# Kernel tuning notes

Hardware: AMD Instinct MI355X
Metric: run time of the kernel (lower is better)

The kernel has to match this reference:

```python
import jax, jax.numpy as jnp
import numpy as np

T, N, E, F, H = 8, 50000, 800000, 128, 128
NHEADS = 4
DH = H // NHEADS


def setup_inputs() -> dict:
    key = jax.random.key(0)
    ks = jax.random.split(key, 24)

    def rn(k, shape, scale=0.05):
        return jax.random.normal(k, shape, dtype=jnp.float32) * scale

    return {
        "xs": rn(ks[0], (T, N, F), 1.0),
        "edge_index": jax.random.randint(ks[1], (T, 2, E), 0, N, dtype=jnp.int32),
        # SAGEConv layers: out = mean_aggr(x_src) @ Wl + x @ Wr + b (bias on lin_l only)
        "Wl1": rn(ks[2], (F, H)), "Wr1": rn(ks[3], (F, H)), "b1": jnp.zeros((H,), jnp.float32),
        "Wl2": rn(ks[4], (H, H)), "Wr2": rn(ks[5], (H, H)), "b2": jnp.zeros((H,), jnp.float32),
        "Wl3": rn(ks[6], (H, H)), "Wr3": rn(ks[7], (H, H)), "b3": jnp.zeros((H,), jnp.float32),
        # MultiheadAttention (applied as x @ W, i.e. W = torch_weight.T)
        "Wq": rn(ks[8], (H, H)), "bq": jnp.zeros((H,), jnp.float32),
        "Wk": rn(ks[9], (H, H)), "bk": jnp.zeros((H,), jnp.float32),
        "Wv": rn(ks[10], (H, H)), "bv": jnp.zeros((H,), jnp.float32),
        "Wo": rn(ks[11], (H, H)), "bo": jnp.zeros((H,), jnp.float32),
        # MLP head
        "Wh1": rn(ks[12], (H, H // 2)), "bh1": jnp.zeros((H // 2,), jnp.float32),
        "Wh2": rn(ks[13], (H // 2, 1)), "bh2": jnp.zeros((1,), jnp.float32),
    }


def _sage(x, src, dst, Wl, Wr, b):
    # gather messages from source nodes, mean-aggregate at destinations
    msg = x[src]                                               # [E, F]
    ssum = jax.ops.segment_sum(msg, dst, num_segments=N)       # [N, F]
    cnt = jax.ops.segment_sum(jnp.ones((msg.shape[0],), x.dtype), dst, num_segments=N)
    agg = ssum / jnp.maximum(cnt, 1.0)[:, None]
    return agg @ Wl + x @ Wr + b


def reference(xs, edge_index, Wl1, Wr1, b1, Wl2, Wr2, b2, Wl3, Wr3, b3,
              Wq, bq, Wk, bk, Wv, bv, Wo, bo, Wh1, bh1, Wh2, bh2):
    def step(_, xe):
        x, ei = xe
        src, dst = ei[0], ei[1]
        h = jax.nn.relu(_sage(x, src, dst, Wl1, Wr1, b1))  # dropout = identity (eval)
        h = jax.nn.relu(_sage(h, src, dst, Wl2, Wr2, b2))
        h = jax.nn.relu(_sage(h, src, dst, Wl3, Wr3, b3))
        return None, h.mean(axis=0)                        # mean pool over nodes -> [H]

    _, pooled = jax.lax.scan(step, None, (xs, edge_index))  # [T, H]

    seq = pooled[None]                                      # [1, T, H]
    q = (seq @ Wq + bq).reshape(1, T, NHEADS, DH).transpose(0, 2, 1, 3)
    k = (seq @ Wk + bk).reshape(1, T, NHEADS, DH).transpose(0, 2, 1, 3)
    v = (seq @ Wv + bv).reshape(1, T, NHEADS, DH).transpose(0, 2, 1, 3)
    scale = jnp.float32(1.0 / np.sqrt(DH))
    attn = jax.nn.softmax(jnp.einsum('bhqd,bhkd->bhqk', q, k) * scale, axis=-1)
    o = jnp.einsum('bhqk,bhkd->bhqd', attn, v).transpose(0, 2, 1, 3).reshape(1, T, H)
    o = o @ Wo + bo                                         # [1, T, H]

    z = o[:, -1, :]                                         # [1, H] (last timestep)
    h1 = jax.nn.relu(z @ Wh1 + bh1)
    logits = jax.nn.sigmoid(h1 @ Wh2 + bh2)                 # [1, 1]
    return logits.squeeze(-1)                               # [1]
```

## Files before the change

kernel.cpp:

```cpp
#include <hip/hip_runtime.h>
#include <math.h>

#define TT 8
#define NN 50000
#define EE 800000
#define FF 128
#define HH 128

#define NB 98
#define BSHIFT 9
#define CAP 14336
#define RS 16384

typedef __attribute__((ext_vector_type(8))) short short8;
typedef __attribute__((ext_vector_type(4))) float f32x4;
typedef __attribute__((ext_vector_type(2))) float f32x2;
typedef unsigned char uchar;

__device__ inline unsigned bf16pack(float x) {
    unsigned u = __float_as_uint(x);
    return (u + 0x7fffu + ((u >> 16) & 1u)) >> 16;
}
__device__ inline unsigned pack2bf16_trunc(float lo, float hi) {
    return (__float_as_uint(hi) & 0xffff0000u) | (__float_as_uint(lo) >> 16);
}


__global__ __launch_bounds__(256) void cast_x_kernel(const float4* __restrict__ in,
                                                     int* __restrict__ out, long n4) {
    long i = (long)blockIdx.x * 256 + threadIdx.x;
    if (i < n4) {
        float4 v = in[i];
        int w = __builtin_amdgcn_cvt_pk_fp8_f32(v.x, v.y, 0, false);
        w = __builtin_amdgcn_cvt_pk_fp8_f32(v.z, v.w, w, true);
        out[i] = w;
    }
}

__global__ __launch_bounds__(256) void wprep_kernel(const float* __restrict__ Wl,
                                                    const float* __restrict__ Wr,
                                                    ushort* __restrict__ Bt) {
    int n = blockIdx.x;
    int k = threadIdx.x;
    float v = (k < 128) ? Wl[k * HH + n] : Wr[(k - 128) * HH + n];
    Bt[n * 256 + k] = (ushort)bf16pack(v);
}


__global__ __launch_bounds__(256) void partA_kernel(const int* __restrict__ ei,
                                                    int* __restrict__ bucketCursor,
                                                    uint2* __restrict__ pairs) {
    __shared__ int hist[NB];
    __shared__ int base[NB];
    int t = blockIdx.y, tid = threadIdx.x;
    const int* src = ei + (size_t)t * 2 * EE;
    const int* dst = src + EE;
    int e0 = blockIdx.x * 2048;
    int s[8], d[8];
#pragma unroll
    for (int k = 0; k < 8; k++) {
        int e = e0 + k * 256 + tid;
        bool ok = e < EE;
        s[k] = ok ? src[e] : -1;
        d[k] = ok ? dst[e] : -1;
    }
    if (tid < NB) hist[tid] = 0;
    __syncthreads();
#pragma unroll
    for (int k = 0; k < 8; k++)
        if (d[k] >= 0) atomicAdd(&hist[d[k] >> BSHIFT], 1);
    __syncthreads();
    if (tid < NB) {
        base[tid] = atomicAdd(&bucketCursor[t * NB + tid], hist[tid]);
        hist[tid] = 0;
    }
    __syncthreads();
#pragma unroll
    for (int k = 0; k < 8; k++)
        if (d[k] >= 0) {
            int b = d[k] >> BSHIFT;
            int idx = base[b] + atomicAdd(&hist[b], 1);
            if (idx < CAP)
                pairs[((size_t)t * NB + b) * RS + idx] = make_uint2((unsigned)s[k], (unsigned)d[k]);
        }
}

__global__ void bscan_kernel(const int* __restrict__ bucketCursor,
                             int* __restrict__ bucketBase) {
    int t = threadIdx.x;
    if (t < TT) {
        int run = 0;
        for (int b = 0; b < NB; b++) {
            bucketBase[t * NB + b] = run;
            int c = bucketCursor[t * NB + b];
            run += (c > CAP ? CAP : c);
        }
    }
}

__global__ __launch_bounds__(256) void partB_kernel(const uint2* __restrict__ pairs,
                                                    const int* __restrict__ bucketCursor,
                                                    const int* __restrict__ bucketBase,
                                                    int* __restrict__ cnt,
                                                    int* __restrict__ rowstart,
                                                    int* __restrict__ srcs_sorted) {
    __shared__ int hist[512];
    __shared__ int offs[512];
    __shared__ int sh2[256];
    __shared__ int staged[CAP];
    int t = blockIdx.y, b = blockIdx.x, tid = threadIdx.x;
    int n0 = b << BSHIFT;
    int nn = NN - n0; if (nn > 512) nn = 512;
    int cb = bucketCursor[t * NB + b]; if (cb > CAP) cb = CAP;
    int ebase = bucketBase[t * NB + b];
    const uint2* P = pairs + ((size_t)t * NB + b) * RS;

    hist[tid] = 0; hist[tid + 256] = 0;
    __syncthreads();
    for (int i = tid; i < cb; i += 256) atomicAdd(&hist[(int)P[i].y - n0], 1);
    __syncthreads();
    int a0 = hist[2 * tid], a1 = hist[2 * tid + 1];
    sh2[tid] = a0 + a1;
    __syncthreads();
    for (int off = 1; off < 256; off <<= 1) {
        int v = (tid >= off) ? sh2[tid - off] : 0;
        __syncthreads();
        sh2[tid] += v;
        __syncthreads();
    }
    int excl = sh2[tid] - (a0 + a1);
    offs[2 * tid] = excl;
    offs[2 * tid + 1] = excl + a0;
    __syncthreads();
    for (int i = tid; i < nn; i += 256) {
        cnt[(size_t)t * NN + n0 + i] = hist[i];
        rowstart[(size_t)t * NN + n0 + i] = ebase + offs[i];
    }
    __syncthreads();
    hist[tid] = offs[tid]; hist[tid + 256] = offs[tid + 256];
    __syncthreads();
    for (int i = tid; i < cb; i += 256) {
        uint2 p = P[i];
        int slot = atomicAdd(&hist[(int)p.y - n0], 1);
        staged[slot] = (int)p.x;
    }
    __syncthreads();
    int* outp = srcs_sorted + (size_t)t * EE + ebase;
    for (int i = tid; i < cb; i += 256) outp[i] = staged[i];
}

__global__ __launch_bounds__(256) void agg_kernel(const uchar* __restrict__ xin,
                                                  const int* __restrict__ srcs_sorted,
                                                  const int* __restrict__ rowstart,
                                                  const int* __restrict__ cnt,
                                                  uchar* __restrict__ aggq) {
    int node = blockIdx.x * 4 + (threadIdx.x >> 6);
    if (node >= NN) return;
    int lane = threadIdx.x & 63;
    int quad = lane >> 4, l15 = lane & 15;
    int rs = rowstart[node];
    int c = cnt[node];
    const uint2* x2 = (const uint2*)xin;
    float a0 = 0.f, a1 = 0.f, a2 = 0.f, a3 = 0.f, a4 = 0.f, a5 = 0.f, a6 = 0.f, a7 = 0.f;
    int j = quad;
    for (; j + 4 < c; j += 8) {
        int s0 = srcs_sorted[rs + j];
        int s1 = srcs_sorted[rs + j + 4];
        uint2 v0 = x2[(size_t)s0 * 16 + l15];
        uint2 v1 = x2[(size_t)s1 * 16 + l15];
        f32x2 p;
        p = __builtin_amdgcn_cvt_pk_f32_fp8((int)v0.x, false); a0 += p.x; a1 += p.y;
        p = __builtin_amdgcn_cvt_pk_f32_fp8((int)v0.x, true);  a2 += p.x; a3 += p.y;
        p = __builtin_amdgcn_cvt_pk_f32_fp8((int)v0.y, false); a4 += p.x; a5 += p.y;
        p = __builtin_amdgcn_cvt_pk_f32_fp8((int)v0.y, true);  a6 += p.x; a7 += p.y;
        p = __builtin_amdgcn_cvt_pk_f32_fp8((int)v1.x, false); a0 += p.x; a1 += p.y;
        p = __builtin_amdgcn_cvt_pk_f32_fp8((int)v1.x, true);  a2 += p.x; a3 += p.y;
        p = __builtin_amdgcn_cvt_pk_f32_fp8((int)v1.y, false); a4 += p.x; a5 += p.y;
        p = __builtin_amdgcn_cvt_pk_f32_fp8((int)v1.y, true);  a6 += p.x; a7 += p.y;
    }
    if (j < c) {
        uint2 v0 = x2[(size_t)srcs_sorted[rs + j] * 16 + l15];
        f32x2 p;
        p = __builtin_amdgcn_cvt_pk_f32_fp8((int)v0.x, false); a0 += p.x; a1 += p.y;
        p = __builtin_amdgcn_cvt_pk_f32_fp8((int)v0.x, true);  a2 += p.x; a3 += p.y;
        p = __builtin_amdgcn_cvt_pk_f32_fp8((int)v0.y, false); a4 += p.x; a5 += p.y;
        p = __builtin_amdgcn_cvt_pk_f32_fp8((int)v0.y, true);  a6 += p.x; a7 += p.y;
    }
#pragma unroll
    for (int o = 16; o <= 32; o <<= 1) {
        a0 += __shfl_xor(a0, o, 64);
        a1 += __shfl_xor(a1, o, 64);
        a2 += __shfl_xor(a2, o, 64);
        a3 += __shfl_xor(a3, o, 64);
        a4 += __shfl_xor(a4, o, 64);
        a5 += __shfl_xor(a5, o, 64);
        a6 += __shfl_xor(a6, o, 64);
        a7 += __shfl_xor(a7, o, 64);
    }
    if (quad == 0) {
        float inv = 1.0f / (float)(c > 0 ? c : 1);
        int w0 = __builtin_amdgcn_cvt_pk_fp8_f32(a0 * inv, a1 * inv, 0, false);
        w0 = __builtin_amdgcn_cvt_pk_fp8_f32(a2 * inv, a3 * inv, w0, true);
        int w1 = __builtin_amdgcn_cvt_pk_fp8_f32(a4 * inv, a5 * inv, 0, false);
        w1 = __builtin_amdgcn_cvt_pk_fp8_f32(a6 * inv, a7 * inv, w1, true);
        ((uint2*)aggq)[(size_t)node * 16 + l15] = make_uint2((unsigned)w0, (unsigned)w1);
    }
}

__global__ __launch_bounds__(256) void gemm_mfma_kernel(const uchar* __restrict__ AaggF,
                                                        const uchar* __restrict__ AxF,
                                                        const ushort* __restrict__ Bt,
                                                        const float* __restrict__ bias,
                                                        uchar* __restrict__ outF) {
    extern __shared__ char smem[];
    ushort* As = (ushort*)smem;
    ushort* Bs = (ushort*)(smem + 128 * 72 * 2);
    uchar* Cs = (uchar*)smem;

    size_t toff = (size_t)blockIdx.y * NN * HH;
    const uchar* Aagg = AaggF + toff;
    const uchar* Ax = AxF + toff;
    uchar* out = outF + toff;

    int tid = threadIdx.x;
    int row0 = blockIdx.x * 128;
    int lane = tid & 63, wave = tid >> 6;
    int wm = wave >> 1, wn = wave & 1;
    int l15 = lane & 15, quad = lane >> 4;

    f32x4 acc[4][4];
#pragma unroll
    for (int i = 0; i < 4; i++)
#pragma unroll
        for (int j = 0; j < 4; j++) acc[i][j] = (f32x4){0.f, 0.f, 0.f, 0.f};

    int srow = tid >> 1;
    int cb = (tid & 1) * 32;
    int grow = row0 + srow;

    for (int s = 0; s < 4; s++) {
        const uchar* Asrc = (s < 2) ? Aagg : Ax;
        int acol = (s & 1) * 64 + cb;
        uint4 r0 = make_uint4(0u, 0u, 0u, 0u), r1 = r0;
        if (grow < NN) {
            const uchar* ap = Asrc + (size_t)grow * HH + acol;
            r0 = *(const uint4*)ap;
            r1 = *(const uint4*)(ap + 16);
        }
        const ushort* bp = Bt + srow * 256 + s * 64 + cb;
        uint4 bv[4];
#pragma unroll
        for (int c = 0; c < 4; c++) bv[c] = *(const uint4*)(bp + c * 8);

        unsigned w[8] = {r0.x, r0.y, r0.z, r0.w, r1.x, r1.y, r1.z, r1.w};
        unsigned u[16];
#pragma unroll
        for (int wi = 0; wi < 8; wi++) {
            f32x2 lo = __builtin_amdgcn_cvt_pk_f32_fp8((int)w[wi], false);
            f32x2 hi = __builtin_amdgcn_cvt_pk_f32_fp8((int)w[wi], true);
            u[2 * wi] = pack2bf16_trunc(lo.x, lo.y);
            u[2 * wi + 1] = pack2bf16_trunc(hi.x, hi.y);
        }
        __syncthreads();
#pragma unroll
        for (int c = 0; c < 4; c++)
            *(uint4*)&As[srow * 72 + cb + c * 8] =
                make_uint4(u[4 * c], u[4 * c + 1], u[4 * c + 2], u[4 * c + 3]);
#pragma unroll
        for (int c = 0; c < 4; c++) *(uint4*)&Bs[srow * 72 + cb + c * 8] = bv[c];
        __syncthreads();
#pragma unroll
        for (int ks = 0; ks < 2; ks++) {
            int k0 = ks * 32 + quad * 8;
            short8 a[4], b[4];
#pragma unroll
            for (int i = 0; i < 4; i++)
                a[i] = *(const short8*)&As[(wm * 64 + i * 16 + l15) * 72 + k0];
#pragma unroll
            for (int j = 0; j < 4; j++)
                b[j] = *(const short8*)&Bs[(wn * 64 + j * 16 + l15) * 72 + k0];
#pragma unroll
            for (int i = 0; i < 4; i++)
#pragma unroll
                for (int j = 0; j < 4; j++)
                    acc[i][j] = __builtin_amdgcn_mfma_f32_16x16x32_bf16(a[i], b[j], acc[i][j], 0, 0, 0);
        }
    }
    __syncthreads();

#pragma unroll
    for (int i = 0; i < 4; i++)
#pragma unroll
        for (int j = 0; j < 4; j++) {
            int col = wn * 64 + j * 16 + l15;
            float bb = bias[col];
#pragma unroll
            for (int r = 0; r < 4; r++) {
                int rl = wm * 64 + i * 16 + quad * 4 + r;
                float v = fmaxf(acc[i][j][r] + bb, 0.f);
                int pk = __builtin_amdgcn_cvt_pk_fp8_f32(v, 0.f, 0, false);
                Cs[rl * 144 + col] = (uchar)(pk & 0xff);
            }
        }
    __syncthreads();

    int orow = tid >> 1;
    int ocb = (tid & 1) * 64;
    if (row0 + orow < NN) {
#pragma unroll
        for (int c = 0; c < 4; c++)
            *(uint4*)&out[(size_t)(row0 + orow) * HH + ocb + c * 16] =
                *(const uint4*)&Cs[orow * 144 + ocb + c * 16];
    }
}

__global__ __launch_bounds__(256) void pool_kernel(const uchar* __restrict__ hF,
                                                   float* __restrict__ pooled) {
    int t = blockIdx.y;
    const unsigned* h = (const unsigned*)(hF + (size_t)t * NN * HH);
    int tid = threadIdx.x;
    int wave = tid >> 6, lane = tid & 63;
    int fw = lane & 31;
    int rh = lane >> 5;
    float s0 = 0.f, s1 = 0.f, s2 = 0.f, s3 = 0.f;
    for (int r = blockIdx.x * 8 + wave * 2 + rh; r < NN; r += gridDim.x * 8) {
        unsigned u = h[(size_t)r * 32 + fw];
        f32x2 lo = __builtin_amdgcn_cvt_pk_f32_fp8((int)u, false);
        f32x2 hi = __builtin_amdgcn_cvt_pk_f32_fp8((int)u, true);
        s0 += lo.x; s1 += lo.y; s2 += hi.x; s3 += hi.y;
    }
    s0 += __shfl_xor(s0, 32, 64);
    s1 += __shfl_xor(s1, 32, 64);
    s2 += __shfl_xor(s2, 32, 64);
    s3 += __shfl_xor(s3, 32, 64);
    if (lane < 32) {
        const float inv = 1.0f / (float)NN;
        atomicAdd(&pooled[t * HH + fw * 4 + 0], s0 * inv);
        atomicAdd(&pooled[t * HH + fw * 4 + 1], s1 * inv);
        atomicAdd(&pooled[t * HH + fw * 4 + 2], s2 * inv);
        atomicAdd(&pooled[t * HH + fw * 4 + 3], s3 * inv);
    }
}

__global__ __launch_bounds__(256) void head_kernel(const float* __restrict__ pooled,
                                                   const float* __restrict__ Wq, const float* __restrict__ bq,
                                                   const float* __restrict__ Wk, const float* __restrict__ bk,
                                                   const float* __restrict__ Wv, const float* __restrict__ bv,
                                                   const float* __restrict__ Wo, const float* __restrict__ bo,
                                                   const float* __restrict__ Wh1, const float* __restrict__ bh1,
                                                   const float* __restrict__ Wh2, const float* __restrict__ bh2,
                                                   float* __restrict__ out) {
    __shared__ float seq[TT * HH];
    __shared__ float kb[TT * HH];
    __shared__ float vbuf[TT * HH];
    __shared__ float q7[HH];
    __shared__ float sc[4][8];
    __shared__ float zb[HH];
    __shared__ float ob[HH];
    __shared__ float h1b[64];
    int tid = threadIdx.x;
    for (int i = tid; i < TT * HH; i += 256) seq[i] = pooled[i];
    __syncthreads();
    for (int i = tid; i < TT * HH; i += 256) {
        int t = i >> 7, h = i & 127;
        float sk = bk[h], sv = bv[h];
        for (int j = 0; j < HH; j++) {
            float s = seq[t * HH + j];
            sk += s * Wk[j * HH + h];
            sv += s * Wv[j * HH + h];
        }
        kb[i] = sk;
        vbuf[i] = sv;
    }
    if (tid < HH) {
        float sq = bq[tid];
        for (int j = 0; j < HH; j++) sq += seq[7 * HH + j] * Wq[j * HH + tid];
        q7[tid] = sq;
    }
    __syncthreads();
    if (tid < 32) {
        int g = tid >> 3, tt = tid & 7;
        float s = 0.f;
        for (int d = 0; d < 32; d++) s += q7[g * 32 + d] * kb[tt * HH + g * 32 + d];
        sc[g][tt] = s * 0.1767766952966369f;
    }
    __syncthreads();
    if (tid < 4) {
        float m = -1e30f;
        for (int i = 0; i < 8; i++) m = fmaxf(m, sc[tid][i]);
        float e[8], sum = 0.f;
        for (int i = 0; i < 8; i++) { e[i] = expf(sc[tid][i] - m); sum += e[i]; }
        for (int i = 0; i < 8; i++) sc[tid][i] = e[i] / sum;
    }
    __syncthreads();
    if (tid < HH) {
        int g = tid >> 5;
        float s = 0.f;
        for (int t = 0; t < 8; t++) s += sc[g][t] * vbuf[t * HH + tid];
        zb[tid] = s;
    }
    __syncthreads();
    if (tid < HH) {
        float s = bo[tid];
        for (int j = 0; j < HH; j++) s += zb[j] * Wo[j * HH + tid];
        ob[tid] = s;
    }
    __syncthreads();
    if (tid < 64) {
        float s = bh1[tid];
        for (int j = 0; j < HH; j++) s += ob[j] * Wh1[j * 64 + tid];
        h1b[tid] = fmaxf(s, 0.f);
    }
    __syncthreads();
    if (tid == 0) {
        float s = bh2[0];
        for (int j = 0; j < 64; j++) s += h1b[j] * Wh2[j];
        out[0] = 1.0f / (1.0f + expf(-s));
    }
}


extern "C" void kernel_launch(void* const* d_in, const int* in_sizes, int n_in,
                              void* d_out, int out_size, void* d_ws, size_t ws_size,
                              hipStream_t stream) {
    const float* xs = (const float*)d_in[0];
    const int* ei = (const int*)d_in[1];
    const float* Wl1 = (const float*)d_in[2];
    const float* Wr1 = (const float*)d_in[3];
    const float* b1 = (const float*)d_in[4];
    const float* Wl2 = (const float*)d_in[5];
    const float* Wr2 = (const float*)d_in[6];
    const float* b2 = (const float*)d_in[7];
    const float* Wl3 = (const float*)d_in[8];
    const float* Wr3 = (const float*)d_in[9];
    const float* b3 = (const float*)d_in[10];
    const float* Wq = (const float*)d_in[11];
    const float* bq = (const float*)d_in[12];
    const float* Wk = (const float*)d_in[13];
    const float* bk = (const float*)d_in[14];
    const float* Wv = (const float*)d_in[15];
    const float* bv = (const float*)d_in[16];
    const float* Wo = (const float*)d_in[17];
    const float* bo = (const float*)d_in[18];
    const float* Wh1 = (const float*)d_in[19];
    const float* bh1 = (const float*)d_in[20];
    const float* Wh2 = (const float*)d_in[21];
    const float* bh2 = (const float*)d_in[22];

    size_t off = 0;
    char* base = (char*)d_ws;
    auto carve = [&](size_t bytes) -> char* {
        char* p = base + off;
        off += (bytes + 255) & ~(size_t)255;
        return p;
    };
    int* cnt = (int*)carve((size_t)TT * NN * 4);
    int* rowstart = (int*)carve((size_t)TT * NN * 4);
    int* srcs_sorted = (int*)carve((size_t)TT * EE * 4);
    int* bucketCursor = (int*)carve((size_t)TT * NB * 4);
    int* bucketBase = (int*)carve((size_t)TT * NB * 4);
    uint2* pairs = (uint2*)carve((size_t)TT * NB * RS * 8);
    uchar* xq = (uchar*)carve((size_t)TT * NN * HH);
    uchar* aggq = (uchar*)carve((size_t)TT * NN * HH);
    uchar* h1q = (uchar*)carve((size_t)TT * NN * HH);
    uchar* h2q = (uchar*)carve((size_t)TT * NN * HH);
    ushort* Bt1 = (ushort*)carve((size_t)128 * 256 * 2);
    ushort* Bt2 = (ushort*)carve((size_t)128 * 256 * 2);
    ushort* Bt3 = (ushort*)carve((size_t)128 * 256 * 2);
    float* pooled = (float*)carve((size_t)TT * HH * 4);

    hipMemsetAsync(pooled, 0, (size_t)TT * HH * 4, stream);
    hipMemsetAsync(bucketCursor, 0, (size_t)TT * NB * 4, stream);

    long n4 = (long)TT * NN * FF / 4;
    cast_x_kernel<<<(int)((n4 + 255) / 256), 256, 0, stream>>>((const float4*)xs, (int*)xq, n4);
    wprep_kernel<<<128, 256, 0, stream>>>(Wl1, Wr1, Bt1);
    wprep_kernel<<<128, 256, 0, stream>>>(Wl2, Wr2, Bt2);
    wprep_kernel<<<128, 256, 0, stream>>>(Wl3, Wr3, Bt3);

    partA_kernel<<<dim3((EE + 2047) / 2048, TT), 256, 0, stream>>>(ei, bucketCursor, pairs);
    bscan_kernel<<<1, 64, 0, stream>>>(bucketCursor, bucketBase);
    partB_kernel<<<dim3(NB, TT), 256, 0, stream>>>(pairs, bucketCursor, bucketBase,
                                                   cnt, rowstart, srcs_sorted);

    const int gemmGrid = (NN + 127) / 128;
    const int aggGrid = (NN + 3) / 4;
    const int gemmLds = 128 * 72 * 2 * 2;

    for (int t = 0; t < TT; t++)
        agg_kernel<<<aggGrid, 256, 0, stream>>>(xq + (size_t)t * NN * HH,
                                                srcs_sorted + (size_t)t * EE,
                                                rowstart + (size_t)t * NN,
                                                cnt + (size_t)t * NN,
                                                aggq + (size_t)t * NN * HH);
    gemm_mfma_kernel<<<dim3(gemmGrid, TT), 256, gemmLds, stream>>>(aggq, xq, Bt1, b1, h1q);
    for (int t = 0; t < TT; t++)
        agg_kernel<<<aggGrid, 256, 0, stream>>>(h1q + (size_t)t * NN * HH,
                                                srcs_sorted + (size_t)t * EE,
                                                rowstart + (size_t)t * NN,
                                                cnt + (size_t)t * NN,
                                                aggq + (size_t)t * NN * HH);
    gemm_mfma_kernel<<<dim3(gemmGrid, TT), 256, gemmLds, stream>>>(aggq, h1q, Bt2, b2, h2q);
    for (int t = 0; t < TT; t++)
        agg_kernel<<<aggGrid, 256, 0, stream>>>(h2q + (size_t)t * NN * HH,
                                                srcs_sorted + (size_t)t * EE,
                                                rowstart + (size_t)t * NN,
                                                cnt + (size_t)t * NN,
                                                aggq + (size_t)t * NN * HH);
    gemm_mfma_kernel<<<dim3(gemmGrid, TT), 256, gemmLds, stream>>>(aggq, h2q, Bt3, b3, h1q);

    pool_kernel<<<dim3(64, TT), 256, 0, stream>>>(h1q, pooled);

    head_kernel<<<1, 256, 0, stream>>>(pooled, Wq, bq, Wk, bk, Wv, bv, Wo, bo,
                                       Wh1, bh1, Wh2, bh2, (float*)d_out);
}
```

Baseline: 1.392 ms.

## Compress edge indices to 16-bit, batch agg launches over timesteps, split feature halves

```diff
diff --git a/kernel.cpp b/kernel.cpp
--- a/kernel.cpp
+++ b/kernel.cpp
@@ -37,19 +37,23 @@
     }
 }
 
-__global__ __launch_bounds__(256) void wprep_kernel(const float* __restrict__ Wl,
-                                                    const float* __restrict__ Wr,
+__global__ __launch_bounds__(256) void wprep_kernel(const float* __restrict__ Wl1, const float* __restrict__ Wr1,
+                                                    const float* __restrict__ Wl2, const float* __restrict__ Wr2,
+                                                    const float* __restrict__ Wl3, const float* __restrict__ Wr3,
                                                     ushort* __restrict__ Bt) {
+    int l = blockIdx.y;
+    const float* Wl = (l == 0) ? Wl1 : (l == 1) ? Wl2 : Wl3;
+    const float* Wr = (l == 0) ? Wr1 : (l == 1) ? Wr2 : Wr3;
     int n = blockIdx.x;
     int k = threadIdx.x;
     float v = (k < 128) ? Wl[k * HH + n] : Wr[(k - 128) * HH + n];
-    Bt[n * 256 + k] = (ushort)bf16pack(v);
+    Bt[(size_t)l * 128 * 256 + n * 256 + k] = (ushort)bf16pack(v);
 }
 
 
 __global__ __launch_bounds__(256) void partA_kernel(const int* __restrict__ ei,
                                                     int* __restrict__ bucketCursor,
-                                                    uint2* __restrict__ pairs) {
+                                                    unsigned* __restrict__ pairs) {
     __shared__ int hist[NB];
     __shared__ int base[NB];
     int t = blockIdx.y, tid = threadIdx.x;
@@ -81,7 +85,8 @@
             int b = d[k] >> BSHIFT;
             int idx = base[b] + atomicAdd(&hist[b], 1);
             if (idx < CAP)
-                pairs[((size_t)t * NB + b) * RS + idx] = make_uint2((unsigned)s[k], (unsigned)d[k]);
+                pairs[((size_t)t * NB + b) * RS + idx] =
+                    (unsigned)s[k] | ((unsigned)(d[k] & 511) << 16);
         }
 }
 
@@ -98,26 +103,26 @@
     }
 }
 
-__global__ __launch_bounds__(256) void partB_kernel(const uint2* __restrict__ pairs,
+__global__ __launch_bounds__(256) void partB_kernel(const unsigned* __restrict__ pairs,
                                                     const int* __restrict__ bucketCursor,
                                                     const int* __restrict__ bucketBase,
-                                                    int* __restrict__ cnt,
                                                     int* __restrict__ rowstart,
-                                                    int* __restrict__ srcs_sorted) {
+                                                    ushort* __restrict__ srcs_sorted) {
     __shared__ int hist[512];
     __shared__ int offs[512];
     __shared__ int sh2[256];
-    __shared__ int staged[CAP];
+    __shared__ ushort staged[CAP];
     int t = blockIdx.y, b = blockIdx.x, tid = threadIdx.x;
     int n0 = b << BSHIFT;
     int nn = NN - n0; if (nn > 512) nn = 512;
     int cb = bucketCursor[t * NB + b]; if (cb > CAP) cb = CAP;
     int ebase = bucketBase[t * NB + b];
-    const uint2* P = pairs + ((size_t)t * NB + b) * RS;
+    const unsigned* P = pairs + ((size_t)t * NB + b) * RS;
+    int* rsp = rowstart + (size_t)t * (NN + 1);
 
     hist[tid] = 0; hist[tid + 256] = 0;
     __syncthreads();
-    for (int i = tid; i < cb; i += 256) atomicAdd(&hist[(int)P[i].y - n0], 1);
+    for (int i = tid; i < cb; i += 256) atomicAdd(&hist[P[i] >> 16], 1);
     __syncthreads();
     int a0 = hist[2 * tid], a1 = hist[2 * tid + 1];
     sh2[tid] = a0 + a1;
@@ -132,59 +137,73 @@
     offs[2 * tid] = excl;
     offs[2 * tid + 1] = excl + a0;
     __syncthreads();
-    for (int i = tid; i < nn; i += 256) {
-        cnt[(size_t)t * NN + n0 + i] = hist[i];
-        rowstart[(size_t)t * NN + n0 + i] = ebase + offs[i];
-    }
+    for (int i = tid; i < nn; i += 256) rsp[n0 + i] = ebase + offs[i];
+    if (b == NB - 1 && tid == 0) rsp[NN] = ebase + cb;
     __syncthreads();
     hist[tid] = offs[tid]; hist[tid + 256] = offs[tid + 256];
     __syncthreads();
     for (int i = tid; i < cb; i += 256) {
-        uint2 p = P[i];
-        int slot = atomicAdd(&hist[(int)p.y - n0], 1);
-        staged[slot] = (int)p.x;
-    }
-    __syncthreads();
-    int* outp = srcs_sorted + (size_t)t * EE + ebase;
+        unsigned p = P[i];
+        int slot = atomicAdd(&hist[p >> 16], 1);
+        staged[slot] = (ushort)(p & 0xffffu);
+    }
+    __syncthreads();
+    ushort* outp = srcs_sorted + (size_t)t * EE + ebase;
     for (int i = tid; i < cb; i += 256) outp[i] = staged[i];
 }
 
-__global__ __launch_bounds__(256) void agg_kernel(const uchar* __restrict__ xin,
-                                                  const int* __restrict__ srcs_sorted,
-                                                  const int* __restrict__ rowstart,
-                                                  const int* __restrict__ cnt,
-                                                  uchar* __restrict__ aggq) {
-    int node = blockIdx.x * 4 + (threadIdx.x >> 6);
+__global__ __launch_bounds__(256) void agg_kernel(const uchar* __restrict__ xqF,
+                                                  const ushort* __restrict__ srcsF,
+                                                  const int* __restrict__ rsF,
+                                                  uchar* __restrict__ aggF) {
+    int t = blockIdx.y;
+    int half = blockIdx.x & 1;
+    int node = (blockIdx.x >> 1) * 4 + (threadIdx.x >> 6);
     if (node >= NN) return;
+    const unsigned* x = (const unsigned*)(xqF + (size_t)t * NN * HH) + half * 16;
+    const ushort* srcs = srcsF + (size_t)t * EE;
+    const int* rs = rsF + (size_t)t * (NN + 1);
     int lane = threadIdx.x & 63;
     int quad = lane >> 4, l15 = lane & 15;
-    int rs = rowstart[node];
-    int c = cnt[node];
-    const uint2* x2 = (const uint2*)xin;
-    float a0 = 0.f, a1 = 0.f, a2 = 0.f, a3 = 0.f, a4 = 0.f, a5 = 0.f, a6 = 0.f, a7 = 0.f;
+    int r0 = rs[node];
+    int c = rs[node + 1] - r0;
+    float a0 = 0.f, a1 = 0.f, a2 = 0.f, a3 = 0.f;
     int j = quad;
+    for (; j + 12 < c; j += 16) {
+        int s0 = srcs[r0 + j];
+        int s1 = srcs[r0 + j + 4];
+        int s2 = srcs[r0 + j + 8];
+        int s3 = srcs[r0 + j + 12];
+        unsigned v0 = x[(size_t)s0 * 32 + l15];
+        unsigned v1 = x[(size_t)s1 * 32 + l15];
+        unsigned v2 = x[(size_t)s2 * 32 + l15];
+        unsigned v3 = x[(size_t)s3 * 32 + l15];
+        f32x2 p;
+        p = __builtin_amdgcn_cvt_pk_f32_fp8((int)v0, false); a0 += p.x; a1 += p.y;
+        p = __builtin_amdgcn_cvt_pk_f32_fp8((int)v0, true);  a2 += p.x; a3 += p.y;
+        p = __builtin_amdgcn_cvt_pk_f32_fp8((int)v1, false); a0 += p.x; a1 += p.y;
+        p = __builtin_amdgcn_cvt_pk_f32_fp8((int)v1, true);  a2 += p.x; a3 += p.y;
+        p = __builtin_amdgcn_cvt_pk_f32_fp8((int)v2, false); a0 += p.x; a1 += p.y;
+        p = __builtin_amdgcn_cvt_pk_f32_fp8((int)v2, true);  a2 += p.x; a3 += p.y;
+        p = __builtin_amdgcn_cvt_pk_f32_fp8((int)v3, false); a0 += p.x; a1 += p.y;
+        p = __builtin_amdgcn_cvt_pk_f32_fp8((int)v3, true);  a2 += p.x; a3 += p.y;
+    }
     for (; j + 4 < c; j += 8) {
-        int s0 = srcs_sorted[rs + j];
-        int s1 = srcs_sorted[rs + j + 4];
-        uint2 v0 = x2[(size_t)s0 * 16 + l15];
-        uint2 v1 = x2[(size_t)s1 * 16 + l15];
+        int s0 = srcs[r0 + j];
+        int s1 = srcs[r0 + j + 4];
+        unsigned v0 = x[(size_t)s0 * 32 + l15];
+        unsigned v1 = x[(size_t)s1 * 32 + l15];
         f32x2 p;
-        p = __builtin_amdgcn_cvt_pk_f32_fp8((int)v0.x, false); a0 += p.x; a1 += p.y;
-        p = __builtin_amdgcn_cvt_pk_f32_fp8((int)v0.x, true);  a2 += p.x; a3 += p.y;
-        p = __builtin_amdgcn_cvt_pk_f32_fp8((int)v0.y, false); a4 += p.x; a5 += p.y;
-        p = __builtin_amdgcn_cvt_pk_f32_fp8((int)v0.y, true);  a6 += p.x; a7 += p.y;
-        p = __builtin_amdgcn_cvt_pk_f32_fp8((int)v1.x, false); a0 += p.x; a1 += p.y;
-        p = __builtin_amdgcn_cvt_pk_f32_fp8((int)v1.x, true);  a2 += p.x; a3 += p.y;
-        p = __builtin_amdgcn_cvt_pk_f32_fp8((int)v1.y, false); a4 += p.x; a5 += p.y;
-        p = __builtin_amdgcn_cvt_pk_f32_fp8((int)v1.y, true);  a6 += p.x; a7 += p.y;
+        p = __builtin_amdgcn_cvt_pk_f32_fp8((int)v0, false); a0 += p.x; a1 += p.y;
+        p = __builtin_amdgcn_cvt_pk_f32_fp8((int)v0, true);  a2 += p.x; a3 += p.y;
+        p = __builtin_amdgcn_cvt_pk_f32_fp8((int)v1, false); a0 += p.x; a1 += p.y;
+        p = __builtin_amdgcn_cvt_pk_f32_fp8((int)v1, true);  a2 += p.x; a3 += p.y;
     }
     if (j < c) {
-        uint2 v0 = x2[(size_t)srcs_sorted[rs + j] * 16 + l15];
+        unsigned v0 = x[(size_t)srcs[r0 + j] * 32 + l15];
         f32x2 p;
-        p = __builtin_amdgcn_cvt_pk_f32_fp8((int)v0.x, false); a0 += p.x; a1 += p.y;
-        p = __builtin_amdgcn_cvt_pk_f32_fp8((int)v0.x, true);  a2 += p.x; a3 += p.y;
-        p = __builtin_amdgcn_cvt_pk_f32_fp8((int)v0.y, false); a4 += p.x; a5 += p.y;
-        p = __builtin_amdgcn_cvt_pk_f32_fp8((int)v0.y, true);  a6 += p.x; a7 += p.y;
+        p = __builtin_amdgcn_cvt_pk_f32_fp8((int)v0, false); a0 += p.x; a1 += p.y;
+        p = __builtin_amdgcn_cvt_pk_f32_fp8((int)v0, true);  a2 += p.x; a3 += p.y;
     }
 #pragma unroll
     for (int o = 16; o <= 32; o <<= 1) {
@@ -192,18 +211,12 @@
         a1 += __shfl_xor(a1, o, 64);
         a2 += __shfl_xor(a2, o, 64);
         a3 += __shfl_xor(a3, o, 64);
-        a4 += __shfl_xor(a4, o, 64);
-        a5 += __shfl_xor(a5, o, 64);
-        a6 += __shfl_xor(a6, o, 64);
-        a7 += __shfl_xor(a7, o, 64);
     }
     if (quad == 0) {
         float inv = 1.0f / (float)(c > 0 ? c : 1);
-        int w0 = __builtin_amdgcn_cvt_pk_fp8_f32(a0 * inv, a1 * inv, 0, false);
-        w0 = __builtin_amdgcn_cvt_pk_fp8_f32(a2 * inv, a3 * inv, w0, true);
-        int w1 = __builtin_amdgcn_cvt_pk_fp8_f32(a4 * inv, a5 * inv, 0, false);
-        w1 = __builtin_amdgcn_cvt_pk_fp8_f32(a6 * inv, a7 * inv, w1, true);
-        ((uint2*)aggq)[(size_t)node * 16 + l15] = make_uint2((unsigned)w0, (unsigned)w1);
+        int w = __builtin_amdgcn_cvt_pk_fp8_f32(a0 * inv, a1 * inv, 0, false);
+        w = __builtin_amdgcn_cvt_pk_fp8_f32(a2 * inv, a3 * inv, w, true);
+        ((unsigned*)(aggF + (size_t)t * NN * HH))[node * 32 + half * 16 + l15] = (unsigned)w;
     }
 }
 
@@ -454,19 +467,16 @@
         off += (bytes + 255) & ~(size_t)255;
         return p;
     };
-    int* cnt = (int*)carve((size_t)TT * NN * 4);
-    int* rowstart = (int*)carve((size_t)TT * NN * 4);
-    int* srcs_sorted = (int*)carve((size_t)TT * EE * 4);
+    int* rowstart = (int*)carve((size_t)TT * (NN + 1) * 4);
+    ushort* srcs_sorted = (ushort*)carve((size_t)TT * EE * 2);
     int* bucketCursor = (int*)carve((size_t)TT * NB * 4);
     int* bucketBase = (int*)carve((size_t)TT * NB * 4);
-    uint2* pairs = (uint2*)carve((size_t)TT * NB * RS * 8);
+    unsigned* pairs = (unsigned*)carve((size_t)TT * NB * RS * 4);
     uchar* xq = (uchar*)carve((size_t)TT * NN * HH);
     uchar* aggq = (uchar*)carve((size_t)TT * NN * HH);
     uchar* h1q = (uchar*)carve((size_t)TT * NN * HH);
     uchar* h2q = (uchar*)carve((size_t)TT * NN * HH);
-    ushort* Bt1 = (ushort*)carve((size_t)128 * 256 * 2);
-    ushort* Bt2 = (ushort*)carve((size_t)128 * 256 * 2);
-    ushort* Bt3 = (ushort*)carve((size_t)128 * 256 * 2);
+    ushort* Bt = (ushort*)carve((size_t)3 * 128 * 256 * 2);
     float* pooled = (float*)carve((size_t)TT * HH * 4);
 
     hipMemsetAsync(pooled, 0, (size_t)TT * HH * 4, stream);
@@ -474,40 +484,23 @@
 
     long n4 = (long)TT * NN * FF / 4;
     cast_x_kernel<<<(int)((n4 + 255) / 256), 256, 0, stream>>>((const float4*)xs, (int*)xq, n4);
-    wprep_kernel<<<128, 256, 0, stream>>>(Wl1, Wr1, Bt1);
-    wprep_kernel<<<128, 256, 0, stream>>>(Wl2, Wr2, Bt2);
-    wprep_kernel<<<128, 256, 0, stream>>>(Wl3, Wr3, Bt3);
+    wprep_kernel<<<dim3(128, 3), 256, 0, stream>>>(Wl1, Wr1, Wl2, Wr2, Wl3, Wr3, Bt);
 
     partA_kernel<<<dim3((EE + 2047) / 2048, TT), 256, 0, stream>>>(ei, bucketCursor, pairs);
     bscan_kernel<<<1, 64, 0, stream>>>(bucketCursor, bucketBase);
     partB_kernel<<<dim3(NB, TT), 256, 0, stream>>>(pairs, bucketCursor, bucketBase,
-                                                   cnt, rowstart, srcs_sorted);
+                                                   rowstart, srcs_sorted);
 
     const int gemmGrid = (NN + 127) / 128;
-    const int aggGrid = (NN + 3) / 4;
+    const int aggGridX = 25000;
     const int gemmLds = 128 * 72 * 2 * 2;
 
-    for (int t = 0; t < TT; t++)
-        agg_kernel<<<aggGrid, 256, 0, stream>>>(xq + (size_t)t * NN * HH,
-                                                srcs_sorted + (size_t)t * EE,
-                                                rowstart + (size_t)t * NN,
-                                                cnt + (size_t)t * NN,
-                                                aggq + (size_t)t * NN * HH);
-    gemm_mfma_kernel<<<dim3(gemmGrid, TT), 256, gemmLds, stream>>>(aggq, xq, Bt1, b1, h1q);
-    for (int t = 0; t < TT; t++)
-        agg_kernel<<<aggGrid, 256, 0, stream>>>(h1q + (size_t)t * NN * HH,
-                                                srcs_sorted + (size_t)t * EE,
-                                                rowstart + (size_t)t * NN,
-                                                cnt + (size_t)t * NN,
-                                                aggq + (size_t)t * NN * HH);
-    gemm_mfma_kernel<<<dim3(gemmGrid, TT), 256, gemmLds, stream>>>(aggq, h1q, Bt2, b2, h2q);
-    for (int t = 0; t < TT; t++)
-        agg_kernel<<<aggGrid, 256, 0, stream>>>(h2q + (size_t)t * NN * HH,
-                                                srcs_sorted + (size_t)t * EE,
-                                                rowstart + (size_t)t * NN,
-                                                cnt + (size_t)t * NN,
-                                                aggq + (size_t)t * NN * HH);
-    gemm_mfma_kernel<<<dim3(gemmGrid, TT), 256, gemmLds, stream>>>(aggq, h2q, Bt3, b3, h1q);
+    agg_kernel<<<dim3(aggGridX, TT), 256, 0, stream>>>(xq, srcs_sorted, rowstart, aggq);
+    gemm_mfma_kernel<<<dim3(gemmGrid, TT), 256, gemmLds, stream>>>(aggq, xq, Bt, b1, h1q);
+    agg_kernel<<<dim3(aggGridX, TT), 256, 0, stream>>>(h1q, srcs_sorted, rowstart, aggq);
+    gemm_mfma_kernel<<<dim3(gemmGrid, TT), 256, gemmLds, stream>>>(aggq, h1q, Bt + 128 * 256, b2, h2q);
+    agg_kernel<<<dim3(aggGridX, TT), 256, 0, stream>>>(h2q, srcs_sorted, rowstart, aggq);
+    gemm_mfma_kernel<<<dim3(gemmGrid, TT), 256, gemmLds, stream>>>(aggq, h2q, Bt + 2 * 128 * 256, b3, h1q);
 
     pool_kernel<<<dim3(64, TT), 256, 0, stream>>>(h1q, pooled);
 
```

Result: slower. 1.589 ms (+14.2%).
